# Performance work log

Measured on AMD Instinct MI355X. Metric: run time of the kernel, lower is better.

The kernel has to match this reference:

```python
import jax, jax.numpy as jnp
import numpy as np

SCALES = (3, 5, 7)

def _avg_pool3d_same(x, k):
    # stride-1 avg_pool3d with padding k//2, count_include_pad=True (torch default).
    # For odd k <= dim this preserves the spatial size, so the subsequent
    # F.interpolate to the input size is an exact identity.
    p = k // 2
    s = jax.lax.reduce_window(
        x, 0.0, jax.lax.add,
        window_dimensions=(1, 1, k, k, k),
        window_strides=(1, 1, 1, 1, 1),
        padding=[(0, 0), (0, 0), (p, p), (p, p), (p, p)])
    return s * (1.0 / float(k ** 3))

def setup_inputs() -> dict:
    key = jax.random.key(0)
    k1, k2 = jax.random.split(key)
    B, C, D, H, W = 2, 48, 64, 64, 64
    x = jax.random.normal(k1, (B, C, D, H, W), dtype=jnp.float32)
    fuse_w = jax.random.normal(k2, (1, len(SCALES) * C), dtype=jnp.float32) * 0.05
    fuse_b = jnp.zeros((1,), dtype=jnp.float32)
    return {"x": x, "fuse_w": fuse_w, "fuse_b": fuse_b}

def reference(x, fuse_w, fuse_b):
    # Multi-scale stride-1 average pooling (sizes preserved -> interp is identity)
    pooled = [_avg_pool3d_same(x, k) for k in SCALES]   # each (B, C, D, H, W)
    cat = jnp.concatenate(pooled, axis=1)               # (B, 3C, D, H, W)
    # 1x1x1 conv to a single channel, then sigmoid
    out = jnp.einsum('bcdhw,oc->bodhw', cat, fuse_w) + fuse_b[None, :, None, None, None]
    return jax.nn.sigmoid(out)                          # (B, 1, D, H, W)
```

## Files before the change

kernel.cpp:

```cpp
#include <hip/hip_runtime.h>
#include <math.h>

#define CH       48
#define DIM      64
#define SPATIAL  (DIM * DIM * DIM)
#define NB       2
#define VOL      (NB * SPATIAL)
#define NS       3
#define CSLAB    (SPATIAL / 4)

#define ROWS     4
#define CG       4
#define CPG      (CH / CG)

#define ZT_PLANE 4096
#define DT       4
#define DTH      (DT + 6)
#define NITEM    (NS * DTH * DIM)

typedef float f4 __attribute__((ext_vector_type(4)));

__global__ __launch_bounds__(256) void kA(
        const float* __restrict__ x,
        const float* __restrict__ fw,
        float* __restrict__ zt) {
    __shared__ float sw[NS * CH];
    __shared__ f4 part[CG][NS][ROWS][16];
    __shared__ f4 red[NS][ROWS][16];
    const int tid = threadIdx.x;
    if (tid < NS * CH) sw[tid] = fw[tid];
    __syncthreads();

    const int lw   = tid & 15;
    const int lr   = (tid >> 4) & 3;
    const int cg   = tid >> 6;
    const int row0 = blockIdx.x * ROWS;
    const int b    = row0 >> 12;
    const int dh   = (row0 & 4095) + lr;

    const f4* xp = (const f4*)x
        + (size_t)(b * CH + cg * CPG) * CSLAB
        + (size_t)dh * 16 + lw;

    f4 a0 = {0,0,0,0}, a1 = {0,0,0,0}, a2 = {0,0,0,0};
    #pragma unroll
    for (int c = 0; c < CPG; ++c) {
        f4 v = __builtin_nontemporal_load(&xp[(size_t)c * CSLAB]);
        const int cc = cg * CPG + c;
        a0 += sw[cc] * v;
        a1 += sw[CH + cc] * v;
        a2 += sw[2 * CH + cc] * v;
    }
    part[cg][0][lr][lw] = a0;
    part[cg][1][lr][lw] = a1;
    part[cg][2][lr][lw] = a2;
    __syncthreads();

    const int s = tid >> 6;
    if (tid < 192) {
        red[s][lr][lw] = part[0][s][lr][lw] + part[1][s][lr][lw]
                       + part[2][s][lr][lw] + part[3][s][lr][lw];
    }
    __syncthreads();
    if (tid < 192) {
        const f4 zero = {0,0,0,0};
        f4 m1 = (lw > 0)  ? red[s][lr][lw - 1] : zero;
        f4 m0 = red[s][lr][lw];
        f4 p1 = (lw < 15) ? red[s][lr][lw + 1] : zero;
        float f[12] = {m1.x, m1.y, m1.z, m1.w,
                       m0.x, m0.y, m0.z, m0.w,
                       p1.x, p1.y, p1.z, p1.w};
        const int p = s + 1;
        f4 r;
        #pragma unroll
        for (int j = 0; j < 4; ++j) {
            float acc = 0.f;
            #pragma unroll
            for (int i = -3; i <= 3; ++i)
                if (i >= -p && i <= p) acc += f[4 + j + i];
            r[j] = acc;
        }
        ((f4*)zt)[((size_t)(s * NB + b) * 16 + lw) * ZT_PLANE + dh] = r;
    }
}

__global__ __launch_bounds__(256) void kB(
        const float* __restrict__ zt,
        const float* __restrict__ fb,
        float* __restrict__ out) {
    __shared__ f4 tile[NS][DTH][DIM];
    const int tid = threadIdx.x;
    const int bid = blockIdx.x;
    const int w4  = bid & 15;
    const int d0  = ((bid >> 4) & 15) * DT;
    const int b   = bid >> 8;

    const f4* zt4 = (const f4*)zt;
    #pragma unroll
    for (int s = 0; s < NS; ++s) {
        const f4* src = zt4 + ((size_t)(s * NB + b) * 16 + w4) * ZT_PLANE;
        #pragma unroll
        for (int t = 0; t < (DTH * DIM + 255) / 256; ++t) {
            int i = tid + t * 256;
            if (i < DTH * DIM) {
                int dd = i >> 6, h = i & 63;
                int gd = d0 - 3 + dd;
                f4 v = {0,0,0,0};
                if (gd >= 0 && gd < DIM) v = src[gd * 64 + h];
                tile[s][dd][h] = v;
            }
        }
    }
    __syncthreads();

    f4 acc[(NITEM + 255) / 256];
    #pragma unroll
    for (int t = 0; t < (NITEM + 255) / 256; ++t) {
        int j = tid + t * 256;
        f4 a = {0,0,0,0};
        if (j < NITEM) {
            int s   = j / (DTH * DIM);
            int rem = j - s * (DTH * DIM);
            int dd  = rem >> 6, h = rem & 63;
            int p   = s + 1;
            int lo  = h - p; if (lo < 0)  lo = 0;
            int hi  = h + p; if (hi > 63) hi = 63;
            for (int hh = lo; hh <= hi; ++hh) a += tile[s][dd][hh];
        }
        acc[t] = a;
    }
    __syncthreads();
    #pragma unroll
    for (int t = 0; t < (NITEM + 255) / 256; ++t) {
        int j = tid + t * 256;
        if (j < NITEM) {
            int s   = j / (DTH * DIM);
            int rem = j - s * (DTH * DIM);
            tile[s][rem >> 6][rem & 63] = acc[t];
        }
    }
    __syncthreads();

    const float inv[NS] = {1.f / 27.f, 1.f / 125.f, 1.f / 343.f};
    const float bias = fb[0];
    const int ddp = tid >> 6, h = tid & 63;
    const int d   = d0 + ddp;
    f4 a2 = {bias, bias, bias, bias};
    #pragma unroll
    for (int s = 0; s < NS; ++s) {
        int p = s + 1;
        f4 a = {0,0,0,0};
        #pragma unroll
        for (int i = -3; i <= 3; ++i)
            if (i >= -p && i <= p) a += tile[s][ddp + 3 + i][h];
        a2 += a * inv[s];
    }
    f4 r;
    #pragma unroll
    for (int jj = 0; jj < 4; ++jj) r[jj] = 1.f / (1.f + __expf(-a2[jj]));
    __builtin_nontemporal_store(r,
        &((f4*)out)[(size_t)b * (SPATIAL / 4) + (size_t)d * 1024 + h * 16 + w4]);
}

extern "C" void kernel_launch(void* const* d_in, const int* in_sizes, int n_in,
                              void* d_out, int out_size, void* d_ws, size_t ws_size,
                              hipStream_t stream) {
    const float* x  = (const float*)d_in[0];
    const float* fw = (const float*)d_in[1];
    const float* fb = (const float*)d_in[2];
    float* out = (float*)d_out;

    float* zt = (float*)d_ws;

    kA<<<NB * DIM * DIM * DIM / DIM / ROWS * DIM / DIM, 256, 0, stream>>>(x, fw, zt);
    kB<<<NB * 16 * (DIM / DT), 256, 0, stream>>>(zt, fb, out);
}
```

Before: 33.24 us.

## Restructure channel-reduction kernel to per-thread full-channel loops over larger chunks

Kernel A now launches 256 blocks, each covering 32 (d,h) rows. Each thread loops over all 48 channels for two float4 columns, so the cross-channel-group shared-memory reduction and one barrier go away. Results are transposed through a padded shared tile before the W-direction box sums are written. The aim is to cut block count and sync overhead and give each thread more loads in flight. The cost is far fewer blocks (256) to hide memory latency on a large GPU, with a long serial 48-iteration load chain per thread.

```diff
diff --git a/kernel.cpp b/kernel.cpp
--- a/kernel.cpp
+++ b/kernel.cpp
@@ -8,10 +8,7 @@
 #define VOL      (NB * SPATIAL)
 #define NS       3
 #define CSLAB    (SPATIAL / 4)
-
-#define ROWS     4
-#define CG       4
-#define CPG      (CH / CG)
+#define CK_F4    512
 
 #define ZT_PLANE 4096
 #define DT       4
@@ -25,62 +22,63 @@
         const float* __restrict__ fw,
         float* __restrict__ zt) {
     __shared__ float sw[NS * CH];
-    __shared__ f4 part[CG][NS][ROWS][16];
-    __shared__ f4 red[NS][ROWS][16];
+    __shared__ f4 tile[NS][32][17];
     const int tid = threadIdx.x;
     if (tid < NS * CH) sw[tid] = fw[tid];
     __syncthreads();
 
-    const int lw   = tid & 15;
-    const int lr   = (tid >> 4) & 3;
-    const int cg   = tid >> 6;
-    const int row0 = blockIdx.x * ROWS;
-    const int b    = row0 >> 12;
-    const int dh   = (row0 & 4095) + lr;
+    const int b  = blockIdx.x >> 7;
+    const int ck = blockIdx.x & 127;
+    const f4* xb = (const f4*)x + (size_t)b * CH * CSLAB + ck * CK_F4 + tid;
 
-    const f4* xp = (const f4*)x
-        + (size_t)(b * CH + cg * CPG) * CSLAB
-        + (size_t)dh * 16 + lw;
+    f4 a00 = {0,0,0,0}, a01 = {0,0,0,0};
+    f4 a10 = {0,0,0,0}, a11 = {0,0,0,0};
+    f4 a20 = {0,0,0,0}, a21 = {0,0,0,0};
+    #pragma unroll 8
+    for (int c = 0; c < CH; ++c) {
+        f4 v0 = __builtin_nontemporal_load(&xb[(size_t)c * CSLAB]);
+        f4 v1 = __builtin_nontemporal_load(&xb[(size_t)c * CSLAB + 256]);
+        float w0 = sw[c], w1 = sw[CH + c], w2 = sw[2 * CH + c];
+        a00 += w0 * v0; a01 += w0 * v1;
+        a10 += w1 * v0; a11 += w1 * v1;
+        a20 += w2 * v0; a21 += w2 * v1;
+    }
 
-    f4 a0 = {0,0,0,0}, a1 = {0,0,0,0}, a2 = {0,0,0,0};
-    #pragma unroll
-    for (int c = 0; c < CPG; ++c) {
-        f4 v = __builtin_nontemporal_load(&xp[(size_t)c * CSLAB]);
-        const int cc = cg * CPG + c;
-        a0 += sw[cc] * v;
-        a1 += sw[CH + cc] * v;
-        a2 += sw[2 * CH + cc] * v;
-    }
-    part[cg][0][lr][lw] = a0;
-    part[cg][1][lr][lw] = a1;
-    part[cg][2][lr][lw] = a2;
+    const int tr = tid >> 4, tc = tid & 15;
+    tile[0][tr][tc] = a00; tile[0][tr + 16][tc] = a01;
+    tile[1][tr][tc] = a10; tile[1][tr + 16][tc] = a11;
+    tile[2][tr][tc] = a20; tile[2][tr + 16][tc] = a21;
     __syncthreads();
 
-    const int s = tid >> 6;
-    if (tid < 192) {
-        red[s][lr][lw] = part[0][s][lr][lw] + part[1][s][lr][lw]
-                       + part[2][s][lr][lw] + part[3][s][lr][lw];
-    }
-    __syncthreads();
-    if (tid < 192) {
-        const f4 zero = {0,0,0,0};
-        f4 m1 = (lw > 0)  ? red[s][lr][lw - 1] : zero;
-        f4 m0 = red[s][lr][lw];
-        f4 p1 = (lw < 15) ? red[s][lr][lw + 1] : zero;
-        float f[12] = {m1.x, m1.y, m1.z, m1.w,
-                       m0.x, m0.y, m0.z, m0.w,
-                       p1.x, p1.y, p1.z, p1.w};
+    const int r  = tid >> 3;
+    const int k0 = (tid & 7) * 2;
+    const int dh = ck * 32 + r;
+    const f4 zero = {0,0,0,0};
+    f4* zt4 = (f4*)zt;
+    #pragma unroll
+    for (int s = 0; s < NS; ++s) {
+        f4 A = (k0 > 0)  ? tile[s][r][k0 - 1] : zero;
+        f4 B = tile[s][r][k0];
+        f4 C = tile[s][r][k0 + 1];
+        f4 D = (k0 < 14) ? tile[s][r][k0 + 2] : zero;
+        float fa[16] = {A.x, A.y, A.z, A.w, B.x, B.y, B.z, B.w,
+                        C.x, C.y, C.z, C.w, D.x, D.y, D.z, D.w};
         const int p = s + 1;
-        f4 r;
+        f4 r0, r1;
         #pragma unroll
         for (int j = 0; j < 4; ++j) {
-            float acc = 0.f;
+            float s0 = 0.f, s1 = 0.f;
             #pragma unroll
-            for (int i = -3; i <= 3; ++i)
-                if (i >= -p && i <= p) acc += f[4 + j + i];
-            r[j] = acc;
+            for (int i = -3; i <= 3; ++i) {
+                if (i >= -p && i <= p) {
+                    s0 += fa[4 + j + i];
+                    s1 += fa[8 + j + i];
+                }
+            }
+            r0[j] = s0; r1[j] = s1;
         }
-        ((f4*)zt)[((size_t)(s * NB + b) * 16 + lw) * ZT_PLANE + dh] = r;
+        zt4[((size_t)(s * NB + b) * 16 + k0)     * ZT_PLANE + dh] = r0;
+        zt4[((size_t)(s * NB + b) * 16 + k0 + 1) * ZT_PLANE + dh] = r1;
     }
 }
 
@@ -172,6 +170,6 @@
 
     float* zt = (float*)d_ws;
 
-    kA<<<NB * DIM * DIM * DIM / DIM / ROWS * DIM / DIM, 256, 0, stream>>>(x, fw, zt);
+    kA<<<NB * 128, 256, 0, stream>>>(x, fw, zt);
     kB<<<NB * 16 * (DIM / DT), 256, 0, stream>>>(zt, fb, out);
 }
```

New measurement: 34.75 us. +4.5%, slower.
